# Kernel optimization log

Hardware: AMD Instinct MI355X
Metric: run time of the kernel (lower is better)

## Reference

```python
import jax, jax.numpy as jnp
import numpy as np

N_BINS = 10  # matches init_kwargs n_bins

def setup_inputs() -> dict:
    key = jax.random.key(0)
    k1, k2 = jax.random.split(key)
    N, C = 262144, 128
    logits = jax.random.normal(k1, (N, C), dtype=jnp.float32)
    targets = jax.random.randint(k2, (N,), 0, C, dtype=jnp.int64)
    return {"logits": logits, "targets": targets}

def reference(logits, targets):
    # probs / confidence / prediction
    probs = jax.nn.softmax(logits, axis=1)                 # [N, C]
    confidences = jnp.max(probs, axis=1)                   # [N]
    predictions = jnp.argmax(probs, axis=1)                # [N]
    accuracies = (predictions == targets).astype(logits.dtype)

    # bin id for (lower, upper] bins of width 1/N_BINS:
    # conf in (k/N_BINS, (k+1)/N_BINS]  ->  ceil(conf*N_BINS)-1 == k
    bin_ids = jnp.clip(
        jnp.ceil(confidences * N_BINS).astype(jnp.int32) - 1, 0, N_BINS - 1
    )

    n = confidences.shape[0]
    ones = jnp.ones_like(confidences)
    counts = jax.ops.segment_sum(ones, bin_ids, num_segments=N_BINS)        # [B]
    sum_conf = jax.ops.segment_sum(confidences, bin_ids, num_segments=N_BINS)
    sum_acc = jax.ops.segment_sum(accuracies, bin_ids, num_segments=N_BINS)

    safe_counts = jnp.maximum(counts, 1.0)
    avg_conf = sum_conf / safe_counts
    avg_acc = sum_acc / safe_counts
    prop_in_bin = counts / n
    per_bin = jnp.where(counts > 0, jnp.abs(avg_conf - avg_acc) * prop_in_bin, 0.0)
    return jnp.sum(per_bin)
```

## Files before the change

kernel.cpp:

```cpp
#include <hip/hip_runtime.h>
#include <hip/hip_bf16.h>

#define NBINS 10
#define C 128
#define U 4
#define NREP 64
#define REPSTRIDE 32


__global__ __launch_bounds__(256) void ece_main_kernel(
    const float* __restrict__ logits, const int* __restrict__ targets,
    unsigned long long* __restrict__ gbins, int N) {
  __shared__ unsigned long long sbins[3 * NBINS];
  const int tid = threadIdx.x;
  for (int i = tid; i < 3 * NBINS; i += blockDim.x) sbins[i] = 0ull;
  __syncthreads();

  const int lane = tid & 63;
  const int half = lane >> 5;
  const int hl = lane & 31;
  const int wavesPerBlock = blockDim.x >> 6;
  const int wid = blockIdx.x * wavesPerBlock + (tid >> 6);
  const int nwaves = gridDim.x * wavesPerBlock;

  const int npairs = N >> 1;

  for (int p0 = wid * U; p0 < npairs; p0 += nwaves * U) {
    float4 v[U];
    int pp[U];
    #pragma unroll
    for (int u = 0; u < U; ++u) {
      const int p = p0 + u;
      pp[u] = p < npairs ? p : npairs - 1;
      v[u] = *reinterpret_cast<const float4*>(
          logits + (size_t)pp[u] * (2 * C) + half * C + hl * 4);
    }

    float m[U], lm[U];
    int col[U];
    #pragma unroll
    for (int u = 0; u < U; ++u) {
      float mm = v[u].x; int c = 0;
      if (v[u].y > mm) { mm = v[u].y; c = 1; }
      if (v[u].z > mm) { mm = v[u].z; c = 2; }
      if (v[u].w > mm) { mm = v[u].w; c = 3; }
      m[u] = mm; lm[u] = mm; col[u] = (hl << 2) + c;
    }

    #pragma unroll
    for (int off = 1; off <= 16; off <<= 1) {
      #pragma unroll
      for (int u = 0; u < U; ++u) m[u] = fmaxf(m[u], __shfl_xor(m[u], off));
    }

    int wcol[U];
    #pragma unroll
    for (int u = 0; u < U; ++u) {
      const unsigned long long b = __ballot(lm[u] == m[u]);
      const unsigned slice = (unsigned)(b >> (half << 5));
      const int srcl = (half << 5) + (__ffs(slice) - 1);
      wcol[u] = __shfl(col[u], srcl);
    }

    float s[U];
    #pragma unroll
    for (int u = 0; u < U; ++u)
      s[u] = (__expf(v[u].x - m[u]) + __expf(v[u].y - m[u])) +
             (__expf(v[u].z - m[u]) + __expf(v[u].w - m[u]));
    #pragma unroll
    for (int off = 1; off <= 16; off <<= 1) {
      #pragma unroll
      for (int u = 0; u < U; ++u) s[u] += __shfl_xor(s[u], off);
    }

    #pragma unroll
    for (int u = 0; u < U; ++u) {
      if ((p0 + u) < npairs && hl == 0) {
        const float conf = 1.0f / s[u];
        int bin = (int)ceilf(conf * 10.0f) - 1;
        bin = min(max(bin, 0), NBINS - 1);
        const int tgt = targets[pp[u] * 2 + half];
        const unsigned long long acc = (tgt == wcol[u]) ? 1ull : 0ull;
        const unsigned long long confq =
            (unsigned long long)((double)conf * 4294967296.0);
        atomicAdd(&sbins[bin], 1ull);
        atomicAdd(&sbins[NBINS + bin], confq);
        atomicAdd(&sbins[2 * NBINS + bin], acc);
      }
    }
  }

  if ((N & 1) && wid == 0 && half == 0) {
    const int row = N - 1;
    const float4 x = *reinterpret_cast<const float4*>(
        logits + (size_t)row * C + hl * 4);
    float m = x.x; int c = 0;
    if (x.y > m) { m = x.y; c = 1; }
    if (x.z > m) { m = x.z; c = 2; }
    if (x.w > m) { m = x.w; c = 3; }
    const float lmv = m;
    const int col = (hl << 2) + c;
    #pragma unroll
    for (int off = 1; off <= 16; off <<= 1) m = fmaxf(m, __shfl_xor(m, off));
    const unsigned long long b = __ballot(lmv == m);
    const int srcl = __ffs((unsigned)b) - 1;
    const int wcol = __shfl(col, srcl);
    float s = (__expf(x.x - m) + __expf(x.y - m)) +
              (__expf(x.z - m) + __expf(x.w - m));
    #pragma unroll
    for (int off = 1; off <= 16; off <<= 1) s += __shfl_xor(s, off);
    if (hl == 0) {
      const float conf = 1.0f / s;
      int bin = (int)ceilf(conf * 10.0f) - 1;
      bin = min(max(bin, 0), NBINS - 1);
      const unsigned long long acc = (targets[row] == wcol) ? 1ull : 0ull;
      const unsigned long long confq =
          (unsigned long long)((double)conf * 4294967296.0);
      atomicAdd(&sbins[bin], 1ull);
      atomicAdd(&sbins[NBINS + bin], confq);
      atomicAdd(&sbins[2 * NBINS + bin], acc);
    }
  }

  __syncthreads();
  unsigned long long* rep = gbins + (size_t)(blockIdx.x & (NREP - 1)) * REPSTRIDE;
  for (int i = tid; i < 3 * NBINS; i += blockDim.x) {
    unsigned long long vv = sbins[i];
    if (vv) atomicAdd(&rep[i], vv);
  }
}

__global__ void ece_final_kernel(const unsigned long long* __restrict__ gbins,
                                 float* __restrict__ out, int N) {
  __shared__ unsigned long long tot[3 * NBINS];
  const int t = threadIdx.x;
  if (t < 3 * NBINS) {
    unsigned long long s = 0ull;
    #pragma unroll 8
    for (int r = 0; r < NREP; ++r) s += gbins[(size_t)r * REPSTRIDE + t];
    tot[t] = s;
  }
  __syncthreads();
  float per = 0.0f;
  if (t < NBINS) {
    const double cnt = (double)tot[t];
    const double sc = (double)tot[NBINS + t] * (1.0 / 4294967296.0);
    const double sa = (double)tot[2 * NBINS + t];
    const double safe = cnt > 0.0 ? cnt : 1.0;
    const double avg_c = sc / safe;
    const double avg_a = sa / safe;
    const double prop = cnt / (double)N;
    per = (cnt > 0.0) ? (float)(fabs(avg_c - avg_a) * prop) : 0.0f;
  }
  #pragma unroll
  for (int off = 1; off < 16; off <<= 1) per += __shfl_xor(per, off);
  if (t == 0) out[0] = per;
}

extern "C" void kernel_launch(void* const* d_in, const int* in_sizes, int n_in,
                              void* d_out, int out_size, void* d_ws, size_t ws_size,
                              hipStream_t stream) {
  const float* logits = (const float*)d_in[0];
  const int* targets = (const int*)d_in[1];
  float* out = (float*)d_out;
  unsigned long long* gbins = (unsigned long long*)d_ws;

  const int N = in_sizes[1];

  hipMemsetAsync(gbins, 0, NREP * REPSTRIDE * sizeof(unsigned long long),
                 stream);

  const int block = 256;
  const int wavesPerBlock = block / 64;
  const int npairs = N >> 1;
  int grid = 2048;
  int maxGrid = (npairs + wavesPerBlock * U - 1) / (wavesPerBlock * U);
  if (grid > maxGrid) grid = maxGrid > 0 ? maxGrid : 1;

  ece_main_kernel<<<grid, block, 0, stream>>>(logits, targets, gbins, N);
  ece_final_kernel<<<1, 64, 0, stream>>>(gbins, out, N);
}
```

Before: 39.09 us.

## Replace global atomic bins and memset with per-block partials and tree reduce

Each block now writes its shared-memory bin totals to a slot-major partial array instead of doing atomic adds into 64 replicated global bins. This removes the hipMemsetAsync launch and the global atomics. The final kernel grows to 1024 threads and reduces each slot across all blocks with 32 lanes and wave shuffles. Target loads are also hoisted so they are issued alongside the logit loads rather than after the reductions. The cost is a larger partial buffer (30 x grid) and a heavier single-block final pass over 2048 entries per slot.

```diff
diff --git a/kernel.cpp b/kernel.cpp
--- a/kernel.cpp
+++ b/kernel.cpp
@@ -4,16 +4,15 @@
 #define NBINS 10
 #define C 128
 #define U 4
-#define NREP 64
-#define REPSTRIDE 32
+#define SLOTS (3 * NBINS)
 
 
 __global__ __launch_bounds__(256) void ece_main_kernel(
     const float* __restrict__ logits, const int* __restrict__ targets,
-    unsigned long long* __restrict__ gbins, int N) {
-  __shared__ unsigned long long sbins[3 * NBINS];
+    unsigned long long* __restrict__ partial, int N) {
+  __shared__ unsigned long long sbins[SLOTS];
   const int tid = threadIdx.x;
-  for (int i = tid; i < 3 * NBINS; i += blockDim.x) sbins[i] = 0ull;
+  for (int i = tid; i < SLOTS; i += blockDim.x) sbins[i] = 0ull;
   __syncthreads();
 
   const int lane = tid & 63;
@@ -28,12 +27,17 @@
   for (int p0 = wid * U; p0 < npairs; p0 += nwaves * U) {
     float4 v[U];
     int pp[U];
+    int tg[U];
     #pragma unroll
     for (int u = 0; u < U; ++u) {
       const int p = p0 + u;
       pp[u] = p < npairs ? p : npairs - 1;
       v[u] = *reinterpret_cast<const float4*>(
           logits + (size_t)pp[u] * (2 * C) + half * C + hl * 4);
+    }
+    if (hl == 0) {
+      #pragma unroll
+      for (int u = 0; u < U; ++u) tg[u] = targets[pp[u] * 2 + half];
     }
 
     float m[U], lm[U];
@@ -79,8 +83,7 @@
         const float conf = 1.0f / s[u];
         int bin = (int)ceilf(conf * 10.0f) - 1;
         bin = min(max(bin, 0), NBINS - 1);
-        const int tgt = targets[pp[u] * 2 + half];
-        const unsigned long long acc = (tgt == wcol[u]) ? 1ull : 0ull;
+        const unsigned long long acc = (tg[u] == wcol[u]) ? 1ull : 0ull;
         const unsigned long long confq =
             (unsigned long long)((double)conf * 4294967296.0);
         atomicAdd(&sbins[bin], 1ull);
@@ -123,38 +126,42 @@
   }
 
   __syncthreads();
-  unsigned long long* rep = gbins + (size_t)(blockIdx.x & (NREP - 1)) * REPSTRIDE;
-  for (int i = tid; i < 3 * NBINS; i += blockDim.x) {
-    unsigned long long vv = sbins[i];
-    if (vv) atomicAdd(&rep[i], vv);
-  }
+  if (tid < SLOTS)
+    partial[(size_t)tid * gridDim.x + blockIdx.x] = sbins[tid];
 }
 
-__global__ void ece_final_kernel(const unsigned long long* __restrict__ gbins,
-                                 float* __restrict__ out, int N) {
-  __shared__ unsigned long long tot[3 * NBINS];
+__global__ __launch_bounds__(1024) void ece_final_kernel(
+    const unsigned long long* __restrict__ partial, float* __restrict__ out,
+    int N, int nblocks) {
+  __shared__ unsigned long long tot[SLOTS];
   const int t = threadIdx.x;
-  if (t < 3 * NBINS) {
+  const int slot = t >> 5;
+  const int j = t & 31;
+  if (slot < SLOTS) {
     unsigned long long s = 0ull;
-    #pragma unroll 8
-    for (int r = 0; r < NREP; ++r) s += gbins[(size_t)r * REPSTRIDE + t];
-    tot[t] = s;
+    const unsigned long long* p = partial + (size_t)slot * nblocks;
+    for (int b = j; b < nblocks; b += 32) s += p[b];
+    #pragma unroll
+    for (int off = 1; off <= 16; off <<= 1)
+      s += __shfl_xor(s, off);
+    if (j == 0) tot[slot] = s;
   }
   __syncthreads();
-  float per = 0.0f;
-  if (t < NBINS) {
-    const double cnt = (double)tot[t];
-    const double sc = (double)tot[NBINS + t] * (1.0 / 4294967296.0);
-    const double sa = (double)tot[2 * NBINS + t];
-    const double safe = cnt > 0.0 ? cnt : 1.0;
-    const double avg_c = sc / safe;
-    const double avg_a = sa / safe;
-    const double prop = cnt / (double)N;
-    per = (cnt > 0.0) ? (float)(fabs(avg_c - avg_a) * prop) : 0.0f;
+  if (t == 0) {
+    double ece = 0.0;
+    #pragma unroll
+    for (int k = 0; k < NBINS; ++k) {
+      const double cnt = (double)tot[k];
+      const double sc = (double)tot[NBINS + k] * (1.0 / 4294967296.0);
+      const double sa = (double)tot[2 * NBINS + k];
+      const double safe = cnt > 0.0 ? cnt : 1.0;
+      const double avg_c = sc / safe;
+      const double avg_a = sa / safe;
+      const double prop = cnt / (double)N;
+      if (cnt > 0.0) ece += fabs(avg_c - avg_a) * prop;
+    }
+    out[0] = (float)ece;
   }
-  #pragma unroll
-  for (int off = 1; off < 16; off <<= 1) per += __shfl_xor(per, off);
-  if (t == 0) out[0] = per;
 }
 
 extern "C" void kernel_launch(void* const* d_in, const int* in_sizes, int n_in,
@@ -163,12 +170,9 @@
   const float* logits = (const float*)d_in[0];
   const int* targets = (const int*)d_in[1];
   float* out = (float*)d_out;
-  unsigned long long* gbins = (unsigned long long*)d_ws;
+  unsigned long long* partial = (unsigned long long*)d_ws;
 
   const int N = in_sizes[1];
-
-  hipMemsetAsync(gbins, 0, NREP * REPSTRIDE * sizeof(unsigned long long),
-                 stream);
 
   const int block = 256;
   const int wavesPerBlock = block / 64;
@@ -177,6 +181,6 @@
   int maxGrid = (npairs + wavesPerBlock * U - 1) / (wavesPerBlock * U);
   if (grid > maxGrid) grid = maxGrid > 0 ? maxGrid : 1;
 
-  ece_main_kernel<<<grid, block, 0, stream>>>(logits, targets, gbins, N);
-  ece_final_kernel<<<1, 64, 0, stream>>>(gbins, out, N);
+  ece_main_kernel<<<grid, block, 0, stream>>>(logits, targets, partial, N);
+  ece_final_kernel<<<1, 1024, 0, stream>>>(partial, out, N, grid);
 }
```

New measurement: 50.25 us. 28.5% more time.
